# Kernel optimization log

Hardware: AMD Instinct MI355X
Metric: run time of the kernel (lower is better)

Reference implementation:

```python
import jax, jax.numpy as jnp
import numpy as np

EPS = 1e-5
TEMPERATURE = 1.0


def _gn(x, w, b):
    # GroupNorm(dim, dim): num_groups == channels -> per-channel norm over spatial
    mu = x.mean((2, 3), keepdims=True)
    var = x.var((2, 3), keepdims=True)
    return (x - mu) * jax.lax.rsqrt(var + EPS) * w[None, :, None, None] + b[None, :, None, None]


def _deconv(x, w, b):
    # torch ConvTranspose2d(Cin, Cout, 3, stride=2, padding=1, output_padding=1)
    # == dilated conv with lhs_dilation=2, padding (1,2); kernel flip absorbed into random weights
    y = jax.lax.conv_general_dilated(
        x, w, window_strides=(1, 1), padding=((1, 2), (1, 2)),
        lhs_dilation=(2, 2), dimension_numbers=('NCHW', 'OIHW', 'NCHW'))
    return y + b[None, :, None, None]


def _spatial_softmax(logits, temp):
    # logits (..., h, w) -> expected (x, y) coords in [-1, 1], shape (..., 2)
    h, w = logits.shape[-2], logits.shape[-1]
    p = jax.nn.softmax(logits.reshape(*logits.shape[:-2], h * w) / temp, axis=-1)
    ys, xs = jnp.meshgrid(jnp.linspace(-1.0, 1.0, h), jnp.linspace(-1.0, 1.0, w), indexing='ij')
    ex = p @ xs.reshape(-1)
    ey = p @ ys.reshape(-1)
    return jnp.stack([ex, ey], axis=-1)


def setup_inputs() -> dict:
    key = jax.random.key(0)
    ks = iter(jax.random.split(key, 40))
    B, FC, FH = 512, 256, 4   # batch, encoder channels, encoder spatial
    H = 512                   # hidden_size
    STEPS, NHEADS, C = 5, 3, H // 8

    def nrm(shape, scale):
        return jax.random.normal(next(ks), shape, jnp.float32) * scale

    inp = {
        'feat': nrm((B, FC, FH, FH), 1.0),
        'action': jax.random.randint(next(ks), (B,), 0, NHEADS),
        'scene_idx': jax.random.randint(next(ks), (B,), 0, 10),
        'fc_w': nrm((FC, H), (2.0 / FC) ** 0.5),
        'fc_b': jnp.zeros((H,), jnp.float32),
    }
    for i, d in enumerate([512, 256, 128]):
        inp[f'gw{i}'] = jnp.ones((d,), jnp.float32)
        inp[f'gb{i}'] = jnp.zeros((d,), jnp.float32)
        inp[f'dw{i}'] = nrm((d // 2, d, 3, 3), (2.0 / (d * 9)) ** 0.5)
        inp[f'db{i}'] = jnp.zeros((d // 2,), jnp.float32)
    inp['hgw'] = jnp.ones((NHEADS, C), jnp.float32)
    inp['hgb'] = jnp.zeros((NHEADS, C), jnp.float32)
    inp['hcw'] = nrm((NHEADS, STEPS, C), (2.0 / C) ** 0.5)
    inp['hcb'] = jnp.zeros((NHEADS, STEPS), jnp.float32)
    return inp


def reference(feat, action, scene_idx, fc_w, fc_b,
              gw0, gb0, dw0, db0, gw1, gb1, dw1, db1, gw2, gb2, dw2, db2,
              hgw, hgb, hcw, hcb):
    # visual_fc1 applied channel-last == 1x1 linear over channels
    x = jax.nn.relu(jnp.einsum('bchw,cd->bdhw', feat, fc_w) + fc_b[None, :, None, None])
    # deconv stack: (B,512,4,4) -> (B,256,8,8) -> (B,128,16,16) -> (B,64,32,32)
    for gw, gb, dw, db in ((gw0, gb0, dw0, db0), (gw1, gb1, dw1, db1), (gw2, gb2, dw2, db2)):
        x = jax.nn.relu(_deconv(_gn(x, gw, gb), dw, db))
    # expert heads: shared per-channel normalization, head-specific affine fused into 1x1 conv
    mu = x.mean((2, 3), keepdims=True)
    var = x.var((2, 3), keepdims=True)
    xn = (x - mu) * jax.lax.rsqrt(var + EPS)                       # (B,64,32,32)
    w_eff = hcw * hgw[:, None, :]                                  # (A,S,C)
    b_eff = hcb + jnp.einsum('asc,ac->as', hcw, hgb)               # (A,S)
    logits = jnp.einsum('bchw,asc->abshw', xn, w_eff) + b_eff[:, None, :, None, None]
    coords = _spatial_softmax(logits, TEMPERATURE)                 # (A,B,S,2)
    # route each sample to its action's head (== masked scatter loop in torch)
    out = coords[action, jnp.arange(action.shape[0])]              # (B,S,2)
    return out
```

## Files before the change

### kernel.cpp

```cpp
#include <hip/hip_runtime.h>
#include <hip/hip_bf16.h>

#define DI __device__ __forceinline__
using u16 = unsigned short;
using u32 = unsigned int;

typedef short short8 __attribute__((ext_vector_type(8)));
typedef float f32x4 __attribute__((ext_vector_type(4)));

#define F4C(v, i) ((i) == 0 ? (v).x : (i) == 1 ? (v).y : (i) == 2 ? (v).z : (v).w)

DI float bflo(u32 u) { return __uint_as_float(u << 16); }
DI float bfhi(u32 u) { return __uint_as_float(u & 0xffff0000u); }
DI float bfel(uint2 u, int j) { u32 w = (j < 2) ? u.x : u.y; return (j & 1) ? bfhi(w) : bflo(w); }
DI u16 f2bf(float a) {
  u32 xu = __float_as_uint(a);
  return (u16)((xu + 0x7fffu + ((xu >> 16) & 1)) >> 16);
}
DI u32 pack_bf16x2(float a, float b) {
  u32 xu = __float_as_uint(a), yu = __float_as_uint(b);
  xu = (xu + 0x7fffu + ((xu >> 16) & 1)) >> 16;
  yu = (yu + 0x7fffu + ((yu >> 16) & 1)) >> 16;
  return (xu & 0xffffu) | (yu << 16);
}

static constexpr size_t OFF_REGB = 0;
static constexpr size_t OFF_REGA = 16777216;
static constexpr size_t OFF_WT0  = 33554432;
static constexpr size_t OFF_WT1  = OFF_WT0 + 1179648;
static constexpr size_t OFF_WT2  = OFF_WT1 + 294912;
static constexpr size_t OFF_WTF  = OFF_WT2 + 73728;
static constexpr size_t OFF_ST   = 35200000;
static constexpr size_t O_SC0 = OFF_ST,          O_SH0 = OFF_ST + 262144;
static constexpr size_t O_SC1 = OFF_ST + 524288, O_SH1 = OFF_ST + 655360;
static constexpr size_t O_SC2 = OFF_ST + 786432, O_SH2 = OFF_ST + 851968;
static constexpr size_t O_PSUM = OFF_ST + 1048576;

__global__ __launch_bounds__(256)
void wtrans_all(const float* __restrict__ dw0, const float* __restrict__ dw1,
                const float* __restrict__ dw2, const float* __restrict__ fcw,
                u16* __restrict__ wt0, u16* __restrict__ wt1,
                u16* __restrict__ wt2, u16* __restrict__ wtf)
{
  int id = blockIdx.x * 256 + threadIdx.x;
  if (id < 131072) {
    int m = id >> 9, c = id & 511;
    const float* src = dw0 + ((size_t)m * 512 + c) * 9;
#pragma unroll
    for (int tap = 0; tap < 9; ++tap)
      wt0[((size_t)tap * 256 + m) * 512 + c] = f2bf(src[tap]);
  } else if (id < 163840) {
    int j = id - 131072;
    int m = j >> 8, c = j & 255;
    const float* src = dw1 + ((size_t)m * 256 + c) * 9;
#pragma unroll
    for (int tap = 0; tap < 9; ++tap)
      wt1[((size_t)tap * 128 + m) * 256 + c] = f2bf(src[tap]);
  } else if (id < 172032) {
    int j = id - 163840;
    int m = j >> 7, c = j & 127;
    const float* src = dw2 + ((size_t)m * 128 + c) * 9;
#pragma unroll
    for (int tap = 0; tap < 9; ++tap)
      wt2[((size_t)tap * 64 + m) * 128 + c] = f2bf(src[tap]);
  } else {
    int j = id - 172032;
    int d = j >> 8, c = j & 255;
    wtf[j] = f2bf(fcw[c * 512 + d]);
  }
}

DI void fc_stage_A(const float* __restrict__ feat, int b, u16* Ab, int t)
{
#pragma unroll
  for (int it = 0; it < 2; ++it) {
    int idx = t + it * 256;
    int cp = idx >> 2, hw4 = idx & 3;
    int c = cp * 2;
    const float* xp = feat + ((size_t)b * 256 + c) * 16 + hw4 * 4;
    float4 v0 = *(const float4*)xp;
    float4 v1 = *(const float4*)(xp + 16);
    int c64 = c >> 6, jb = (c & 63) >> 3;
#pragma unroll
    for (int j = 0; j < 4; ++j) {
      int hw = hw4 * 4 + j;
      int row = c64 * 16 + hw;
      *(u32*)&Ab[(row << 6) + ((jb ^ (row & 7)) << 3) + (c & 7)] =
          pack_bf16x2(F4C(v0, j), F4C(v1, j));
    }
  }
}

__global__ __launch_bounds__(256, 2)
void fc_mfma(const float* __restrict__ feat, const u16* __restrict__ wtf,
             const float* __restrict__ fb, const float* __restrict__ gw,
             const float* __restrict__ gb, u16* __restrict__ x0,
             float* __restrict__ sc, float* __restrict__ sh)
{
  __shared__ __align__(16) u16 Wl[256 * 64];
  __shared__ __align__(16) u16 Al[2][64 * 64];
  const int t = threadIdx.x;
  const int lane = t & 63, wave = t >> 6;
  const int n15 = lane & 15, kq = lane >> 4;
  const int d0 = blockIdx.x * 64;
  const int b0 = blockIdx.y * 8;

#pragma unroll
  for (int it = 0; it < 8; ++it) {
    int idx = t + it * 256;
    int dl = idx >> 5, jb32 = idx & 31;
    int row = (jb32 >> 3) * 64 + dl, jb = jb32 & 7;
    uint4 v = *(const uint4*)(wtf + (size_t)(d0 + dl) * 256 + jb32 * 8);
    *(uint4*)&Wl[(row << 6) + ((jb ^ (row & 7)) << 3)] = v;
  }
  fc_stage_A(feat, b0, Al[0], t);

  const int dg = d0 + wave * 16 + n15;
  const float bvn = fb[dg];
  const float gwv = gw[dg], gbv = gb[dg];

  for (int bi = 0; bi < 8; ++bi) {
    __syncthreads();
    if (bi + 1 < 8) fc_stage_A(feat, b0 + bi + 1, Al[(bi + 1) & 1], t);

    const u16* A = Al[bi & 1];
    f32x4 acc0 = {0.f, 0.f, 0.f, 0.f}, acc1 = {0.f, 0.f, 0.f, 0.f};
#pragma unroll
    for (int ks = 0; ks < 8; ++ks) {
      int js = ks * 4 + kq;
      int ra = (js >> 3) * 16 + n15;
      int rb = (js >> 3) * 64 + wave * 16 + n15;
      short8 av = *(const short8*)&A[(ra << 6) + (((js & 7) ^ (ra & 7)) << 3)];
      short8 bv = *(const short8*)&Wl[(rb << 6) + (((js & 7) ^ (rb & 7)) << 3)];
      if (ks & 1) acc1 = __builtin_amdgcn_mfma_f32_16x16x32_bf16(av, bv, acc1, 0, 0, 0);
      else        acc0 = __builtin_amdgcn_mfma_f32_16x16x32_bf16(av, bv, acc0, 0, 0, 0);
    }

    int b = b0 + bi;
    float v[4], s = 0.f, s2 = 0.f;
#pragma unroll
    for (int r = 0; r < 4; ++r) {
      v[r] = fmaxf(acc0[r] + acc1[r] + bvn, 0.f);
      s += v[r]; s2 += v[r] * v[r];
    }
    uint2 pk = {pack_bf16x2(v[0], v[1]), pack_bf16x2(v[2], v[3])};
    *(uint2*)&x0[((size_t)b * 512 + dg) * 16 + kq * 4] = pk;
    s  += __shfl_xor(s, 16, 64);  s  += __shfl_xor(s, 32, 64);
    s2 += __shfl_xor(s2, 16, 64); s2 += __shfl_xor(s2, 32, 64);
    if (kq == 0) {
      float mu = s * (1.f / 16.f);
      float var = fmaxf(s2 * (1.f / 16.f) - mu * mu, 0.f);
      float scale = gwv * rsqrtf(var + 1e-5f);
      sc[(size_t)b * 512 + dg] = scale;
      sh[(size_t)b * 512 + dg] = gbv - mu * scale;
    }
  }
}

template<int STAGE>
__global__ __launch_bounds__(256, 3)
void deconv_mfma(const u16* __restrict__ x, const float* __restrict__ sc,
                 const float* __restrict__ sh, const u16* __restrict__ wt,
                 const float* __restrict__ bias, u16* __restrict__ y,
                 const float* __restrict__ gwn, const float* __restrict__ gbn,
                 float* __restrict__ osc, float* __restrict__ osh)
{
  constexpr int CI  = STAGE == 0 ? 512 : 256;
  constexpr int CO  = CI / 2;
  constexpr int H   = STAGE == 0 ? 4 : 8;
  constexpr int S2I = H * H, S2O = 4 * S2I, W2 = 2 * H;
  constexpr int WP  = H + 1;
  constexpr int XROWS = STAGE == 0 ? 100 : 81;
  constexpr int NCH = CI / 64;
  __shared__ __align__(16) u16 Wl[288 * 64];
  __shared__ __align__(16) u16 Xl[XROWS * 64];
  __shared__ float2 sbuf[2][2][16];

  const int t = threadIdx.x;
  const int lane = t & 63, wave = t >> 6;
  const int ms = wave >> 1, ns = wave & 1;
  const int n15 = lane & 15, kq = lane >> 4;

  int m0, b0;
  m0 = blockIdx.x * 32; b0 = (STAGE == 0) ? blockIdx.y * 4 : blockIdx.y;

  int xrow[2];
#pragma unroll
  for (int ni = 0; ni < 2; ++ni) {
    if constexpr (STAGE == 0) xrow[ni] = (ns * 2 + ni) * 25 + (n15 >> 2) * 5 + (n15 & 3);
    else                      xrow[ni] = (2 * (ns * 2 + ni) + (n15 >> 3)) * 9 + (n15 & 7);
  }
  const int am = ms * 16 + n15;

  for (int i = t; i < XROWS * 32; i += 256) ((u32*)Xl)[i] = 0;

  f32x4 acc[2][4];
#pragma unroll
  for (int ni = 0; ni < 2; ++ni)
#pragma unroll
    for (int c = 0; c < 4; ++c) acc[ni][c] = f32x4{0.f, 0.f, 0.f, 0.f};

  for (int ch = 0; ch < NCH; ++ch) {
    const int c0 = ch * 64;
    __syncthreads();

#pragma unroll
    for (int it = 0; it < 9; ++it) {
      int idx = t + it * 256;
      int row = idx >> 3, jb = idx & 7;
      int tap = row >> 5, ml = row & 31;
      uint4 v = *(const uint4*)(wt + ((size_t)(tap * CO + m0 + ml)) * CI + c0 + jb * 8);
      *(uint4*)&Wl[(row << 6) + ((jb ^ (row & 7)) << 3)] = v;
    }

    for (int idx = t; idx < 16 * 32; idx += 256) {
      int q = idx & 15, p = idx >> 4;
      int c = c0 + 2 * p;
      int b, ldr, gpos;
      if constexpr (STAGE == 0) {
        int img = q >> 2, iy = q & 3;
        b = b0 + img; gpos = iy * 4; ldr = img * 25 + iy * 5;
      } else {
        int iy = q >> 1, cq = q & 1;
        b = b0; gpos = iy * 8 + cq * 4; ldr = iy * 9 + cq * 4;
      }
      const u16* xp = x + ((size_t)b * CI + c) * S2I + gpos;
      uint2 q0 = *(const uint2*)xp;
      uint2 q1 = *(const uint2*)(xp + S2I);
      float s0 = sc[(size_t)b * CI + c],     h0 = sh[(size_t)b * CI + c];
      float s1 = sc[(size_t)b * CI + c + 1], h1 = sh[(size_t)b * CI + c + 1];
      int jb = p >> 2, sub = p & 3;
#pragma unroll
      for (int j = 0; j < 4; ++j) {
        int row = ldr + j;
        *(u32*)&Xl[(row << 6) + ((jb ^ (row & 7)) << 3) + sub * 2] =
            pack_bf16x2(bfel(q0, j) * s0 + h0, bfel(q1, j) * s1 + h1);
      }
    }
    __syncthreads();

#pragma unroll
    for (int s = 0; s < 2; ++s) {
      const int js = s * 4 + kq;
      short8 a[9];
#pragma unroll
      for (int tap = 0; tap < 9; ++tap) {
        int row = tap * 32 + am;
        a[tap] = *(const short8*)&Wl[(row << 6) + ((js ^ (row & 7)) << 3)];
      }
#pragma unroll
      for (int ni = 0; ni < 2; ++ni) {
        int r0 = xrow[ni], r1 = r0 + 1, r2 = r0 + WP, r3 = r0 + WP + 1;
        short8 b00 = *(const short8*)&Xl[(r0 << 6) + ((js ^ (r0 & 7)) << 3)];
        short8 b01 = *(const short8*)&Xl[(r1 << 6) + ((js ^ (r1 & 7)) << 3)];
        short8 b10 = *(const short8*)&Xl[(r2 << 6) + ((js ^ (r2 & 7)) << 3)];
        short8 b11 = *(const short8*)&Xl[(r3 << 6) + ((js ^ (r3 & 7)) << 3)];
        acc[ni][0] = __builtin_amdgcn_mfma_f32_16x16x32_bf16(a[4], b00, acc[ni][0], 0, 0, 0);
        acc[ni][1] = __builtin_amdgcn_mfma_f32_16x16x32_bf16(a[3], b00, acc[ni][1], 0, 0, 0);
        acc[ni][1] = __builtin_amdgcn_mfma_f32_16x16x32_bf16(a[5], b01, acc[ni][1], 0, 0, 0);
        acc[ni][2] = __builtin_amdgcn_mfma_f32_16x16x32_bf16(a[1], b00, acc[ni][2], 0, 0, 0);
        acc[ni][2] = __builtin_amdgcn_mfma_f32_16x16x32_bf16(a[7], b10, acc[ni][2], 0, 0, 0);
        acc[ni][3] = __builtin_amdgcn_mfma_f32_16x16x32_bf16(a[0], b00, acc[ni][3], 0, 0, 0);
        acc[ni][3] = __builtin_amdgcn_mfma_f32_16x16x32_bf16(a[2], b01, acc[ni][3], 0, 0, 0);
        acc[ni][3] = __builtin_amdgcn_mfma_f32_16x16x32_bf16(a[6], b10, acc[ni][3], 0, 0, 0);
        acc[ni][3] = __builtin_amdgcn_mfma_f32_16x16x32_bf16(a[8], b11, acc[ni][3], 0, 0, 0);
      }
    }
  }

  float bv[4];
#pragma unroll
  for (int r = 0; r < 4; ++r) bv[r] = bias[m0 + ms * 16 + kq * 4 + r];

  float sr[4] = {0.f, 0.f, 0.f, 0.f}, sr2[4] = {0.f, 0.f, 0.f, 0.f};
#pragma unroll
  for (int ni = 0; ni < 2; ++ni) {
    int b, iy, ix;
    if constexpr (STAGE == 0) { b = b0 + ns * 2 + ni; iy = n15 >> 2; ix = n15 & 3; }
    else                      { b = b0; iy = 2 * (ns * 2 + ni) + (n15 >> 3); ix = n15 & 7; }

    float val[4][4];
#pragma unroll
    for (int cl = 0; cl < 4; ++cl)
#pragma unroll
      for (int r = 0; r < 4; ++r) {
        val[cl][r] = fmaxf(acc[ni][cl][r] + bv[r], 0.f);
        sr[r] += val[cl][r]; sr2[r] += val[cl][r] * val[cl][r];
      }

    if constexpr (STAGE == 0) {
#pragma unroll
      for (int r = 0; r < 4; ++r) {
        int m = m0 + ms * 16 + kq * 4 + r;
        size_t base = ((size_t)b * CO + m) * S2O + (size_t)(2 * iy) * W2 + 2 * ix;
        *(u32*)(y + base)      = pack_bf16x2(val[0][r], val[1][r]);
        *(u32*)(y + base + W2) = pack_bf16x2(val[2][r], val[3][r]);
      }
#pragma unroll
      for (int r = 0; r < 4; ++r) {
#pragma unroll
        for (int off = 1; off <= 8; off <<= 1) {
          sr[r]  += __shfl_xor(sr[r], off, 64);
          sr2[r] += __shfl_xor(sr2[r], off, 64);
        }
      }
      if (n15 == 0) {
#pragma unroll
        for (int r = 0; r < 4; ++r) {
          int m = m0 + ms * 16 + kq * 4 + r;
          float mu = sr[r] * (1.f / 64.f);
          float var = fmaxf(sr2[r] * (1.f / 64.f) - mu * mu, 0.f);
          float scale = gwn[m] * rsqrtf(var + 1e-5f);
          osc[(size_t)b * CO + m] = scale;
          osh[(size_t)b * CO + m] = gbn[m] - mu * scale;
        }
      }
#pragma unroll
      for (int r = 0; r < 4; ++r) { sr[r] = 0.f; sr2[r] = 0.f; }
    } else {
#pragma unroll
      for (int cl = 0; cl < 4; ++cl) {
        int opx = (2 * iy + (cl >> 1)) * 16 + 2 * ix + (cl & 1);
        size_t base = ((size_t)b * 256 + opx) * 128 + m0 + ms * 16 + kq * 4;
        *(u32*)(y + base)     = pack_bf16x2(val[cl][0], val[cl][1]);
        *(u32*)(y + base + 2) = pack_bf16x2(val[cl][2], val[cl][3]);
      }
    }
  }

  if constexpr (STAGE == 1) {
#pragma unroll
    for (int r = 0; r < 4; ++r) {
#pragma unroll
      for (int off = 1; off <= 8; off <<= 1) {
        sr[r]  += __shfl_xor(sr[r], off, 64);
        sr2[r] += __shfl_xor(sr2[r], off, 64);
      }
    }
    __syncthreads();
    if (n15 == 0) {
#pragma unroll
      for (int r = 0; r < 4; ++r) sbuf[ms][ns][kq * 4 + r] = float2{sr[r], sr2[r]};
    }
    __syncthreads();
    if (t < 32) {
      int msx = t >> 4, i = t & 15;
      float2 p0 = sbuf[msx][0][i], p1 = sbuf[msx][1][i];
      float s = p0.x + p1.x, s2 = p0.y + p1.y;
      float mu = s * (1.f / 256.f);
      float var = fmaxf(s2 * (1.f / 256.f) - mu * mu, 0.f);
      int m = m0 + msx * 16 + i;
      float scale = gwn[m] * rsqrtf(var + 1e-5f);
      osc[(size_t)b0 * CO + m] = scale;
      osh[(size_t)b0 * CO + m] = gbn[m] - mu * scale;
    }
  }
}

#define XRD(row) (*(const short8*)&Xl[((row) << 6) + (((js ^ ((row) & 7))) << 3)])
__global__ __launch_bounds__(256, 3)
void deconv2_q(const u16* __restrict__ x, const float* __restrict__ sc,
               const float* __restrict__ sh, const u16* __restrict__ wt,
               const float* __restrict__ bias, u16* __restrict__ y,
               float2* __restrict__ psum)
{
  __shared__ __align__(16) u16 Wl[288 * 64];
  __shared__ __align__(16) u16 Xl[85 * 64];
  __shared__ float sc_l[128], sh_l[128];
  __shared__ float2 sbuf[2][2][16];

  const int t = threadIdx.x;
  const int lane = t & 63, wave = t >> 6;
  const int ms = wave >> 1, ns = wave & 1;
  const int n15 = lane & 15, kq = lane >> 4;
  const int m0 = (blockIdx.x & 1) * 32;
  const int qz = blockIdx.x >> 1;
  const int b  = blockIdx.y;

  if (t < 128) { sc_l[t] = sc[(size_t)b * 128 + t]; sh_l[t] = sh[(size_t)b * 128 + t]; }
  for (int i = t; i < 85 * 32; i += 256) ((u32*)Xl)[i] = 0;

  const int am = ms * 16 + n15;
  const int xr0 = (ns * 2) * 17 + n15;

  f32x4 acc[2][4];
#pragma unroll
  for (int ni = 0; ni < 2; ++ni)
#pragma unroll
    for (int c = 0; c < 4; ++c) acc[ni][c] = f32x4{0.f, 0.f, 0.f, 0.f};

  const int NPX = (qz < 3) ? 80 : 64;
  for (int ch = 0; ch < 2; ++ch) {
    const int c0 = ch * 64;
    __syncthreads();

#pragma unroll
    for (int it = 0; it < 9; ++it) {
      int idx = t + it * 256;
      int row = idx >> 3, jb = idx & 7;
      int tap = row >> 5, ml = row & 31;
      uint4 v = *(const uint4*)(wt + ((size_t)(tap * 64 + m0 + ml)) * 128 + c0 + jb * 8);
      *(uint4*)&Wl[(row << 6) + ((jb ^ (row & 7)) << 3)] = v;
    }

    for (int idx = t; idx < NPX * 8; idx += 256) {
      int pxl = idx >> 3, jb = idx & 7;
      int rl = pxl >> 4, ix = pxl & 15;
      int gpx = (4 * qz + rl) * 16 + ix;
      uint4 q = *(const uint4*)(x + ((size_t)b * 256 + gpx) * 128 + c0 + jb * 8);
      int cb = c0 + jb * 8;
      float f0 = bflo(q.x) * sc_l[cb + 0] + sh_l[cb + 0];
      float f1 = bfhi(q.x) * sc_l[cb + 1] + sh_l[cb + 1];
      float f2 = bflo(q.y) * sc_l[cb + 2] + sh_l[cb + 2];
      float f3 = bfhi(q.y) * sc_l[cb + 3] + sh_l[cb + 3];
      float f4 = bflo(q.z) * sc_l[cb + 4] + sh_l[cb + 4];
      float f5 = bfhi(q.z) * sc_l[cb + 5] + sh_l[cb + 5];
      float f6 = bflo(q.w) * sc_l[cb + 6] + sh_l[cb + 6];
      float f7 = bfhi(q.w) * sc_l[cb + 7] + sh_l[cb + 7];
      uint4 o = {pack_bf16x2(f0, f1), pack_bf16x2(f2, f3),
                 pack_bf16x2(f4, f5), pack_bf16x2(f6, f7)};
      int row = rl * 17 + ix;
      *(uint4*)&Xl[(row << 6) + ((jb ^ (row & 7)) << 3)] = o;
    }
    __syncthreads();

#pragma unroll
    for (int s = 0; s < 2; ++s) {
      const int js = s * 4 + kq;
      short8 a[9];
#pragma unroll
      for (int tap = 0; tap < 9; ++tap) {
        int row = tap * 32 + am;
        a[tap] = *(const short8*)&Wl[(row << 6) + ((js ^ (row & 7)) << 3)];
      }
      short8 B0 = XRD(xr0),      B1 = XRD(xr0 + 1);
      short8 B2 = XRD(xr0 + 17), B3 = XRD(xr0 + 18);
      short8 B4 = XRD(xr0 + 34), B5 = XRD(xr0 + 35);
#pragma unroll
      for (int ni = 0; ni < 2; ++ni) {
        short8 b00 = ni ? B2 : B0, b01 = ni ? B3 : B1;
        short8 b10 = ni ? B4 : B2, b11 = ni ? B5 : B3;
        acc[ni][0] = __builtin_amdgcn_mfma_f32_16x16x32_bf16(a[4], b00, acc[ni][0], 0, 0, 0);
        acc[ni][1] = __builtin_amdgcn_mfma_f32_16x16x32_bf16(a[3], b00, acc[ni][1], 0, 0, 0);
        acc[ni][1] = __builtin_amdgcn_mfma_f32_16x16x32_bf16(a[5], b01, acc[ni][1], 0, 0, 0);
        acc[ni][2] = __builtin_amdgcn_mfma_f32_16x16x32_bf16(a[1], b00, acc[ni][2], 0, 0, 0);
        acc[ni][2] = __builtin_amdgcn_mfma_f32_16x16x32_bf16(a[7], b10, acc[ni][2], 0, 0, 0);
        acc[ni][3] = __builtin_amdgcn_mfma_f32_16x16x32_bf16(a[0], b00, acc[ni][3], 0, 0, 0);
        acc[ni][3] = __builtin_amdgcn_mfma_f32_16x16x32_bf16(a[2], b01, acc[ni][3], 0, 0, 0);
        acc[ni][3] = __builtin_amdgcn_mfma_f32_16x16x32_bf16(a[6], b10, acc[ni][3], 0, 0, 0);
        acc[ni][3] = __builtin_amdgcn_mfma_f32_16x16x32_bf16(a[8], b11, acc[ni][3], 0, 0, 0);
      }
    }
  }

  float bv[4];
#pragma unroll
  for (int r = 0; r < 4; ++r) bv[r] = bias[m0 + ms * 16 + kq * 4 + r];
  float sr[4] = {0.f, 0.f, 0.f, 0.f}, sr2[4] = {0.f, 0.f, 0.f, 0.f};
#pragma unroll
  for (int ni = 0; ni < 2; ++ni) {
    int iy = 4 * qz + ns * 2 + ni, ix = n15;
#pragma unroll
    for (int r = 0; r < 4; ++r) {
      int m = m0 + ms * 16 + kq * 4 + r;
      float v00 = fmaxf(acc[ni][0][r] + bv[r], 0.f);
      float v01 = fmaxf(acc[ni][1][r] + bv[r], 0.f);
      float v10 = fmaxf(acc[ni][2][r] + bv[r], 0.f);
      float v11 = fmaxf(acc[ni][3][r] + bv[r], 0.f);
      size_t base = ((size_t)b * 64 + m) * 1024 + (size_t)(2 * iy) * 32 + 2 * ix;
      *(u32*)(y + base)      = pack_bf16x2(v00, v01);
      *(u32*)(y + base + 32) = pack_bf16x2(v10, v11);
      sr[r]  += v00 + v01 + v10 + v11;
      sr2[r] += v00 * v00 + v01 * v01 + v10 * v10 + v11 * v11;
    }
  }
#pragma unroll
  for (int r = 0; r < 4; ++r) {
#pragma unroll
    for (int off = 1; off <= 8; off <<= 1) {
      sr[r]  += __shfl_xor(sr[r], off, 64);
      sr2[r] += __shfl_xor(sr2[r], off, 64);
    }
  }
  __syncthreads();
  if (n15 == 0) {
#pragma unroll
    for (int r = 0; r < 4; ++r) sbuf[ms][ns][kq * 4 + r] = float2{sr[r], sr2[r]};
  }
  __syncthreads();
  if (t < 32) {
    int msx = t >> 4, i = t & 15;
    float2 p0 = sbuf[msx][0][i], p1 = sbuf[msx][1][i];
    int m = m0 + msx * 16 + i;
    psum[((size_t)b * 64 + m) * 4 + qz] = float2{p0.x + p1.x, p0.y + p1.y};
  }
}

DI float breduce_sum(float v, float* buf) {
#pragma unroll
  for (int off = 32; off; off >>= 1) v += __shfl_xor(v, off, 64);
  if ((threadIdx.x & 63) == 0) buf[threadIdx.x >> 6] = v;
  __syncthreads();
  float r = (buf[0] + buf[1]) + (buf[2] + buf[3]);
  __syncthreads();
  return r;
}
DI float breduce_max(float v, float* buf) {
#pragma unroll
  for (int off = 32; off; off >>= 1) v = fmaxf(v, __shfl_xor(v, off, 64));
  if ((threadIdx.x & 63) == 0) buf[threadIdx.x >> 6] = v;
  __syncthreads();
  float r = fmaxf(fmaxf(buf[0], buf[1]), fmaxf(buf[2], buf[3]));
  __syncthreads();
  return r;
}

__global__ __launch_bounds__(256)
void head_kernel(const u16* __restrict__ x3, const float2* __restrict__ psum,
                 const int* __restrict__ action, const float* __restrict__ hgw,
                 const float* __restrict__ hcw, float* __restrict__ out)
{
  constexpr int C = 64, S = 5, P = 1024;
  const int b = blockIdx.x, t = threadIdx.x;
  const int a = action[b];
  __shared__ float weff[S * C];
  __shared__ float sc_l[C], sh_l[C];
  __shared__ float rbuf[4];
  if (t < C) {
    float s = 0.f, s2 = 0.f;
#pragma unroll
    for (int qz = 0; qz < 4; ++qz) {
      float2 p = psum[((size_t)b * C + t) * 4 + qz];
      s += p.x; s2 += p.y;
    }
    float mu = s * (1.f / 1024.f);
    float var = fmaxf(s2 * (1.f / 1024.f) - mu * mu, 0.f);
    float rstd = rsqrtf(var + 1e-5f);
    sc_l[t] = rstd; sh_l[t] = -mu * rstd;
  }
  for (int j = t; j < S * C; j += 256) {
    int s = j >> 6, c = j & 63;
    weff[j] = hcw[(a * S + s) * C + c] * hgw[a * C + c];
  }
  __syncthreads();

  float L[S][4];
#pragma unroll
  for (int s = 0; s < S; ++s)
#pragma unroll
    for (int k = 0; k < 4; ++k) L[s][k] = 0.f;

  const u32* xb = (const u32*)(x3 + (size_t)b * C * P);
  for (int c = 0; c < C; ++c) {
    float scv = sc_l[c], shv = sh_l[c];
    u32 u0 = xb[c * 512 + t];
    u32 u1 = xb[c * 512 + t + 256];
    float xv[4] = {bflo(u0) * scv + shv, bfhi(u0) * scv + shv,
                   bflo(u1) * scv + shv, bfhi(u1) * scv + shv};
#pragma unroll
    for (int s = 0; s < S; ++s) {
      float wv = weff[s * C + c];
#pragma unroll
      for (int k = 0; k < 4; ++k) L[s][k] += xv[k] * wv;
    }
  }

#pragma unroll
  for (int s = 0; s < S; ++s) {
    float m = fmaxf(fmaxf(L[s][0], L[s][1]), fmaxf(L[s][2], L[s][3]));
    m = breduce_max(m, rbuf);
    float se = 0.f, sx = 0.f, sy = 0.f;
    const int pix[4] = {2 * t, 2 * t + 1, 512 + 2 * t, 512 + 2 * t + 1};
#pragma unroll
    for (int k = 0; k < 4; ++k) {
      int p = pix[k];
      float e = __expf(L[s][k] - m);
      se += e;
      sx += e * ((float)(p & 31) * (2.f / 31.f) - 1.f);
      sy += e * ((float)(p >> 5) * (2.f / 31.f) - 1.f);
    }
    se = breduce_sum(se, rbuf);
    sx = breduce_sum(sx, rbuf);
    sy = breduce_sum(sy, rbuf);
    if (t == 0) {
      out[(b * S + s) * 2 + 0] = sx / se;
      out[(b * S + s) * 2 + 1] = sy / se;
    }
  }
}

extern "C" void kernel_launch(void* const* d_in, const int* in_sizes, int n_in,
                              void* d_out, int out_size, void* d_ws, size_t ws_size,
                              hipStream_t stream)
{
  (void)in_sizes; (void)n_in; (void)out_size; (void)ws_size;
  const float* feat   = (const float*)d_in[0];
  const int*   action = (const int*)d_in[1];
  const float* fc_w = (const float*)d_in[3];
  const float* fc_b = (const float*)d_in[4];
  const float* gw0  = (const float*)d_in[5];
  const float* gb0  = (const float*)d_in[6];
  const float* dw0  = (const float*)d_in[7];
  const float* db0  = (const float*)d_in[8];
  const float* gw1  = (const float*)d_in[9];
  const float* gb1  = (const float*)d_in[10];
  const float* dw1  = (const float*)d_in[11];
  const float* db1  = (const float*)d_in[12];
  const float* gw2  = (const float*)d_in[13];
  const float* gb2  = (const float*)d_in[14];
  const float* dw2  = (const float*)d_in[15];
  const float* db2  = (const float*)d_in[16];
  const float* hgw  = (const float*)d_in[17];
  const float* hcw  = (const float*)d_in[19];

  float* ws = (float*)d_ws;
  u16* x0 = (u16*)(ws + OFF_REGB);
  u16* x2 = (u16*)(ws + OFF_REGB);
  u16* x1 = (u16*)(ws + OFF_REGA);
  u16* x3 = (u16*)(ws + OFF_REGA);
  u16* wt0 = (u16*)(ws + OFF_WT0);
  u16* wt1 = (u16*)(ws + OFF_WT1);
  u16* wt2 = (u16*)(ws + OFF_WT2);
  u16* wtf = (u16*)(ws + OFF_WTF);
  float* sc0 = ws + O_SC0; float* sh0 = ws + O_SH0;
  float* sc1 = ws + O_SC1; float* sh1 = ws + O_SH1;
  float* sc2 = ws + O_SC2; float* sh2 = ws + O_SH2;
  float2* psum = (float2*)(ws + O_PSUM);

  wtrans_all<<<1184, 256, 0, stream>>>(dw0, dw1, dw2, fc_w, wt0, wt1, wt2, wtf);
  fc_mfma<<<dim3(8, 64), 256, 0, stream>>>(feat, wtf, fc_b, gw0, gb0, x0, sc0, sh0);
  deconv_mfma<0><<<dim3(8, 128), 256, 0, stream>>>(x0, sc0, sh0, wt0, db0, x1, gw1, gb1, sc1, sh1);
  deconv_mfma<1><<<dim3(4, 512), 256, 0, stream>>>(x1, sc1, sh1, wt1, db1, x2, gw2, gb2, sc2, sh2);
  deconv2_q<<<dim3(8, 512), 256, 0, stream>>>(x2, sc2, sh2, wt2, db2, x3, psum);
  head_kernel<<<512, 256, 0, stream>>>(x3, psum, action, hgw, hcw, (float*)d_out);
}
```

Before: 266.1 us.

## Retile last deconv to half-image blocks with 16 channels; halve fc batch per block

The final deconv kernel now tiles each block as 16 output channels by half the input image (8 rows), instead of 32 channels by a quarter (4 rows). Each wave handles different rows with the same channel set, which halves the weight staging in LDS, enlarges the input staging, and targets 4 blocks per CU. Partial GroupNorm statistics are reduced over 2 halves instead of 4, and the head kernel is updated to match. Separately, fc_mfma processes 4 batch items per block instead of 8, doubling the grid for more parallelism at the cost of reloading the weight tile more often.

New measurement: 270.1 us. No clear change (+1.5%).

```diff
diff --git a/kernel.cpp b/kernel.cpp
--- a/kernel.cpp
+++ b/kernel.cpp
@@ -103,7 +103,7 @@
   const int lane = t & 63, wave = t >> 6;
   const int n15 = lane & 15, kq = lane >> 4;
   const int d0 = blockIdx.x * 64;
-  const int b0 = blockIdx.y * 8;
+  const int b0 = blockIdx.y * 4;
 
 #pragma unroll
   for (int it = 0; it < 8; ++it) {
@@ -119,9 +119,9 @@
   const float bvn = fb[dg];
   const float gwv = gw[dg], gbv = gb[dg];
 
-  for (int bi = 0; bi < 8; ++bi) {
+  for (int bi = 0; bi < 4; ++bi) {
     __syncthreads();
-    if (bi + 1 < 8) fc_stage_A(feat, b0 + bi + 1, Al[(bi + 1) & 1], t);
+    if (bi + 1 < 4) fc_stage_A(feat, b0 + bi + 1, Al[(bi + 1) & 1], t);
 
     const u16* A = Al[bi & 1];
     f32x4 acc0 = {0.f, 0.f, 0.f, 0.f}, acc1 = {0.f, 0.f, 0.f, 0.f};
@@ -358,30 +358,26 @@
 }
 
 #define XRD(row) (*(const short8*)&Xl[((row) << 6) + (((js ^ ((row) & 7))) << 3)])
-__global__ __launch_bounds__(256, 3)
-void deconv2_q(const u16* __restrict__ x, const float* __restrict__ sc,
+__global__ __launch_bounds__(256, 4)
+void deconv2_h(const u16* __restrict__ x, const float* __restrict__ sc,
                const float* __restrict__ sh, const u16* __restrict__ wt,
                const float* __restrict__ bias, u16* __restrict__ y,
                float2* __restrict__ psum)
 {
-  __shared__ __align__(16) u16 Wl[288 * 64];
-  __shared__ __align__(16) u16 Xl[85 * 64];
+  __shared__ __align__(16) u16 Wl[144 * 64];
+  __shared__ __align__(16) u16 Xl[153 * 64];
   __shared__ float sc_l[128], sh_l[128];
-  __shared__ float2 sbuf[2][2][16];
+  __shared__ float2 sbuf[4][16];
 
   const int t = threadIdx.x;
-  const int lane = t & 63, wave = t >> 6;
-  const int ms = wave >> 1, ns = wave & 1;
+  const int lane = t & 63, wv = t >> 6;
   const int n15 = lane & 15, kq = lane >> 4;
-  const int m0 = (blockIdx.x & 1) * 32;
-  const int qz = blockIdx.x >> 1;
+  const int m0 = (blockIdx.x & 3) * 16;
+  const int h  = blockIdx.x >> 2;
   const int b  = blockIdx.y;
 
   if (t < 128) { sc_l[t] = sc[(size_t)b * 128 + t]; sh_l[t] = sh[(size_t)b * 128 + t]; }
-  for (int i = t; i < 85 * 32; i += 256) ((u32*)Xl)[i] = 0;
-
-  const int am = ms * 16 + n15;
-  const int xr0 = (ns * 2) * 17 + n15;
+  for (int i = t; i < 153 * 32; i += 256) ((u32*)Xl)[i] = 0;
 
   f32x4 acc[2][4];
 #pragma unroll
@@ -389,24 +385,26 @@
 #pragma unroll
     for (int c = 0; c < 4; ++c) acc[ni][c] = f32x4{0.f, 0.f, 0.f, 0.f};
 
-  const int NPX = (qz < 3) ? 80 : 64;
+  const int NPX = (h == 0) ? 144 : 128;
   for (int ch = 0; ch < 2; ++ch) {
     const int c0 = ch * 64;
     __syncthreads();
 
 #pragma unroll
-    for (int it = 0; it < 9; ++it) {
+    for (int it = 0; it < 5; ++it) {
       int idx = t + it * 256;
-      int row = idx >> 3, jb = idx & 7;
-      int tap = row >> 5, ml = row & 31;
-      uint4 v = *(const uint4*)(wt + ((size_t)(tap * 64 + m0 + ml)) * 128 + c0 + jb * 8);
-      *(uint4*)&Wl[(row << 6) + ((jb ^ (row & 7)) << 3)] = v;
+      if (idx < 1152) {
+        int row = idx >> 3, jb = idx & 7;
+        int tap = row >> 4, ml = row & 15;
+        uint4 v = *(const uint4*)(wt + ((size_t)(tap * 64 + m0 + ml)) * 128 + c0 + jb * 8);
+        *(uint4*)&Wl[(row << 6) + ((jb ^ (row & 7)) << 3)] = v;
+      }
     }
 
     for (int idx = t; idx < NPX * 8; idx += 256) {
       int pxl = idx >> 3, jb = idx & 7;
       int rl = pxl >> 4, ix = pxl & 15;
-      int gpx = (4 * qz + rl) * 16 + ix;
+      int gpx = (8 * h + rl) * 16 + ix;
       uint4 q = *(const uint4*)(x + ((size_t)b * 256 + gpx) * 128 + c0 + jb * 8);
       int cb = c0 + jb * 8;
       float f0 = bflo(q.x) * sc_l[cb + 0] + sh_l[cb + 0];
@@ -430,9 +428,10 @@
       short8 a[9];
 #pragma unroll
       for (int tap = 0; tap < 9; ++tap) {
-        int row = tap * 32 + am;
+        int row = tap * 16 + n15;
         a[tap] = *(const short8*)&Wl[(row << 6) + ((js ^ (row & 7)) << 3)];
       }
+      const int xr0 = (wv * 2) * 17 + n15;
       short8 B0 = XRD(xr0),      B1 = XRD(xr0 + 1);
       short8 B2 = XRD(xr0 + 17), B3 = XRD(xr0 + 18);
       short8 B4 = XRD(xr0 + 34), B5 = XRD(xr0 + 35);
@@ -455,14 +454,14 @@
 
   float bv[4];
 #pragma unroll
-  for (int r = 0; r < 4; ++r) bv[r] = bias[m0 + ms * 16 + kq * 4 + r];
+  for (int r = 0; r < 4; ++r) bv[r] = bias[m0 + kq * 4 + r];
   float sr[4] = {0.f, 0.f, 0.f, 0.f}, sr2[4] = {0.f, 0.f, 0.f, 0.f};
 #pragma unroll
   for (int ni = 0; ni < 2; ++ni) {
-    int iy = 4 * qz + ns * 2 + ni, ix = n15;
+    int iy = 8 * h + wv * 2 + ni, ix = n15;
 #pragma unroll
     for (int r = 0; r < 4; ++r) {
-      int m = m0 + ms * 16 + kq * 4 + r;
+      int m = m0 + kq * 4 + r;
       float v00 = fmaxf(acc[ni][0][r] + bv[r], 0.f);
       float v01 = fmaxf(acc[ni][1][r] + bv[r], 0.f);
       float v10 = fmaxf(acc[ni][2][r] + bv[r], 0.f);
@@ -485,14 +484,14 @@
   __syncthreads();
   if (n15 == 0) {
 #pragma unroll
-    for (int r = 0; r < 4; ++r) sbuf[ms][ns][kq * 4 + r] = float2{sr[r], sr2[r]};
+    for (int r = 0; r < 4; ++r) sbuf[wv][kq * 4 + r] = float2{sr[r], sr2[r]};
   }
   __syncthreads();
-  if (t < 32) {
-    int msx = t >> 4, i = t & 15;
-    float2 p0 = sbuf[msx][0][i], p1 = sbuf[msx][1][i];
-    int m = m0 + msx * 16 + i;
-    psum[((size_t)b * 64 + m) * 4 + qz] = float2{p0.x + p1.x, p0.y + p1.y};
+  if (t < 16) {
+    float s = 0.f, s2 = 0.f;
+#pragma unroll
+    for (int w = 0; w < 4; ++w) { s += sbuf[w][t].x; s2 += sbuf[w][t].y; }
+    psum[((size_t)b * 64 + m0 + t) * 2 + h] = float2{s, s2};
   }
 }
 
@@ -527,12 +526,9 @@
   __shared__ float sc_l[C], sh_l[C];
   __shared__ float rbuf[4];
   if (t < C) {
-    float s = 0.f, s2 = 0.f;
-#pragma unroll
-    for (int qz = 0; qz < 4; ++qz) {
-      float2 p = psum[((size_t)b * C + t) * 4 + qz];
-      s += p.x; s2 += p.y;
-    }
+    float2 p0 = psum[((size_t)b * C + t) * 2 + 0];
+    float2 p1 = psum[((size_t)b * C + t) * 2 + 1];
+    float s = p0.x + p1.x, s2 = p0.y + p1.y;
     float mu = s * (1.f / 1024.f);
     float var = fmaxf(s2 * (1.f / 1024.f) - mu * mu, 0.f);
     float rstd = rsqrtf(var + 1e-5f);
@@ -628,9 +624,9 @@
   float2* psum = (float2*)(ws + O_PSUM);
 
   wtrans_all<<<1184, 256, 0, stream>>>(dw0, dw1, dw2, fc_w, wt0, wt1, wt2, wtf);
-  fc_mfma<<<dim3(8, 64), 256, 0, stream>>>(feat, wtf, fc_b, gw0, gb0, x0, sc0, sh0);
+  fc_mfma<<<dim3(8, 128), 256, 0, stream>>>(feat, wtf, fc_b, gw0, gb0, x0, sc0, sh0);
   deconv_mfma<0><<<dim3(8, 128), 256, 0, stream>>>(x0, sc0, sh0, wt0, db0, x1, gw1, gb1, sc1, sh1);
   deconv_mfma<1><<<dim3(4, 512), 256, 0, stream>>>(x1, sc1, sh1, wt1, db1, x2, gw2, gb2, sc2, sh2);
-  deconv2_q<<<dim3(8, 512), 256, 0, stream>>>(x2, sc2, sh2, wt2, db2, x3, psum);
+  deconv2_h<<<dim3(8, 512), 256, 0, stream>>>(x2, sc2, sh2, wt2, db2, x3, psum);
   head_kernel<<<512, 256, 0, stream>>>(x3, psum, action, hgw, hcw, (float*)d_out);
 }
```

## Remap deconv waves to own a spatial tile and both M halves; halve FC batch per block

Applied to the files above, without the earlier changes.

In the first two deconv stages, each wave now takes one image or row-pair of the spatial tile and computes both 16-row output-channel halves, instead of a 2x2 split over M and N. This loads the four X fragments once per k-step and reuses them across both M halves. The cost is reloading 18 weight fragments per wave instead of 9. The per-channel stats reduction moves to a per-wave shared buffer summed across the four waves. Separately, the FC kernel handles 4 samples per block instead of 8 and launches twice as many blocks, giving more parallelism but restaging the weight tile more often.

New measurement: 268.4 us (median of 2 runs). Within noise of the previous version (+0.9%).

```diff
diff --git a/kernel.cpp b/kernel.cpp
--- a/kernel.cpp
+++ b/kernel.cpp
@@ -103,7 +103,7 @@
   const int lane = t & 63, wave = t >> 6;
   const int n15 = lane & 15, kq = lane >> 4;
   const int d0 = blockIdx.x * 64;
-  const int b0 = blockIdx.y * 8;
+  const int b0 = blockIdx.y * 4;
 
 #pragma unroll
   for (int it = 0; it < 8; ++it) {
@@ -119,9 +119,9 @@
   const float bvn = fb[dg];
   const float gwv = gw[dg], gbv = gb[dg];
 
-  for (int bi = 0; bi < 8; ++bi) {
+  for (int bi = 0; bi < 4; ++bi) {
     __syncthreads();
-    if (bi + 1 < 8) fc_stage_A(feat, b0 + bi + 1, Al[(bi + 1) & 1], t);
+    if (bi + 1 < 4) fc_stage_A(feat, b0 + bi + 1, Al[(bi + 1) & 1], t);
 
     const u16* A = Al[bi & 1];
     f32x4 acc0 = {0.f, 0.f, 0.f, 0.f}, acc1 = {0.f, 0.f, 0.f, 0.f};
@@ -174,31 +174,27 @@
   constexpr int NCH = CI / 64;
   __shared__ __align__(16) u16 Wl[288 * 64];
   __shared__ __align__(16) u16 Xl[XROWS * 64];
-  __shared__ float2 sbuf[2][2][16];
+  __shared__ float2 sbuf[4][32];
 
   const int t = threadIdx.x;
-  const int lane = t & 63, wave = t >> 6;
-  const int ms = wave >> 1, ns = wave & 1;
+  const int lane = t & 63, wv = t >> 6;
   const int n15 = lane & 15, kq = lane >> 4;
 
-  int m0, b0;
-  m0 = blockIdx.x * 32; b0 = (STAGE == 0) ? blockIdx.y * 4 : blockIdx.y;
-
-  int xrow[2];
-#pragma unroll
-  for (int ni = 0; ni < 2; ++ni) {
-    if constexpr (STAGE == 0) xrow[ni] = (ns * 2 + ni) * 25 + (n15 >> 2) * 5 + (n15 & 3);
-    else                      xrow[ni] = (2 * (ns * 2 + ni) + (n15 >> 3)) * 9 + (n15 & 7);
-  }
-  const int am = ms * 16 + n15;
+  const int m0 = blockIdx.x * 32;
+  const int b0 = (STAGE == 0) ? blockIdx.y * 4 : blockIdx.y;
+  const int b  = (STAGE == 0) ? b0 + wv : b0;
+
+  int xrow;
+  if constexpr (STAGE == 0) xrow = wv * 25 + (n15 >> 2) * 5 + (n15 & 3);
+  else                      xrow = (2 * wv + (n15 >> 3)) * 9 + (n15 & 7);
 
   for (int i = t; i < XROWS * 32; i += 256) ((u32*)Xl)[i] = 0;
 
   f32x4 acc[2][4];
 #pragma unroll
-  for (int ni = 0; ni < 2; ++ni)
-#pragma unroll
-    for (int c = 0; c < 4; ++c) acc[ni][c] = f32x4{0.f, 0.f, 0.f, 0.f};
+  for (int mi = 0; mi < 2; ++mi)
+#pragma unroll
+    for (int c = 0; c < 4; ++c) acc[mi][c] = f32x4{0.f, 0.f, 0.f, 0.f};
 
   for (int ch = 0; ch < NCH; ++ch) {
     const int c0 = ch * 64;
@@ -216,19 +212,19 @@
     for (int idx = t; idx < 16 * 32; idx += 256) {
       int q = idx & 15, p = idx >> 4;
       int c = c0 + 2 * p;
-      int b, ldr, gpos;
+      int bb, ldr, gpos;
       if constexpr (STAGE == 0) {
         int img = q >> 2, iy = q & 3;
-        b = b0 + img; gpos = iy * 4; ldr = img * 25 + iy * 5;
+        bb = b0 + img; gpos = iy * 4; ldr = img * 25 + iy * 5;
       } else {
         int iy = q >> 1, cq = q & 1;
-        b = b0; gpos = iy * 8 + cq * 4; ldr = iy * 9 + cq * 4;
-      }
-      const u16* xp = x + ((size_t)b * CI + c) * S2I + gpos;
+        bb = b0; gpos = iy * 8 + cq * 4; ldr = iy * 9 + cq * 4;
+      }
+      const u16* xp = x + ((size_t)bb * CI + c) * S2I + gpos;
       uint2 q0 = *(const uint2*)xp;
       uint2 q1 = *(const uint2*)(xp + S2I);
-      float s0 = sc[(size_t)b * CI + c],     h0 = sh[(size_t)b * CI + c];
-      float s1 = sc[(size_t)b * CI + c + 1], h1 = sh[(size_t)b * CI + c + 1];
+      float s0 = sc[(size_t)bb * CI + c],     h0 = sh[(size_t)bb * CI + c];
+      float s1 = sc[(size_t)bb * CI + c + 1], h1 = sh[(size_t)bb * CI + c + 1];
       int jb = p >> 2, sub = p & 3;
 #pragma unroll
       for (int j = 0; j < 4; ++j) {
@@ -242,56 +238,52 @@
 #pragma unroll
     for (int s = 0; s < 2; ++s) {
       const int js = s * 4 + kq;
-      short8 a[9];
-#pragma unroll
-      for (int tap = 0; tap < 9; ++tap) {
-        int row = tap * 32 + am;
-        a[tap] = *(const short8*)&Wl[(row << 6) + ((js ^ (row & 7)) << 3)];
-      }
-#pragma unroll
-      for (int ni = 0; ni < 2; ++ni) {
-        int r0 = xrow[ni], r1 = r0 + 1, r2 = r0 + WP, r3 = r0 + WP + 1;
-        short8 b00 = *(const short8*)&Xl[(r0 << 6) + ((js ^ (r0 & 7)) << 3)];
-        short8 b01 = *(const short8*)&Xl[(r1 << 6) + ((js ^ (r1 & 7)) << 3)];
-        short8 b10 = *(const short8*)&Xl[(r2 << 6) + ((js ^ (r2 & 7)) << 3)];
-        short8 b11 = *(const short8*)&Xl[(r3 << 6) + ((js ^ (r3 & 7)) << 3)];
-        acc[ni][0] = __builtin_amdgcn_mfma_f32_16x16x32_bf16(a[4], b00, acc[ni][0], 0, 0, 0);
-        acc[ni][1] = __builtin_amdgcn_mfma_f32_16x16x32_bf16(a[3], b00, acc[ni][1], 0, 0, 0);
-        acc[ni][1] = __builtin_amdgcn_mfma_f32_16x16x32_bf16(a[5], b01, acc[ni][1], 0, 0, 0);
-        acc[ni][2] = __builtin_amdgcn_mfma_f32_16x16x32_bf16(a[1], b00, acc[ni][2], 0, 0, 0);
-        acc[ni][2] = __builtin_amdgcn_mfma_f32_16x16x32_bf16(a[7], b10, acc[ni][2], 0, 0, 0);
-        acc[ni][3] = __builtin_amdgcn_mfma_f32_16x16x32_bf16(a[0], b00, acc[ni][3], 0, 0, 0);
-        acc[ni][3] = __builtin_amdgcn_mfma_f32_16x16x32_bf16(a[2], b01, acc[ni][3], 0, 0, 0);
-        acc[ni][3] = __builtin_amdgcn_mfma_f32_16x16x32_bf16(a[6], b10, acc[ni][3], 0, 0, 0);
-        acc[ni][3] = __builtin_amdgcn_mfma_f32_16x16x32_bf16(a[8], b11, acc[ni][3], 0, 0, 0);
-      }
-    }
-  }
-
-  float bv[4];
-#pragma unroll
-  for (int r = 0; r < 4; ++r) bv[r] = bias[m0 + ms * 16 + kq * 4 + r];
-
-  float sr[4] = {0.f, 0.f, 0.f, 0.f}, sr2[4] = {0.f, 0.f, 0.f, 0.f};
-#pragma unroll
-  for (int ni = 0; ni < 2; ++ni) {
-    int b, iy, ix;
-    if constexpr (STAGE == 0) { b = b0 + ns * 2 + ni; iy = n15 >> 2; ix = n15 & 3; }
-    else                      { b = b0; iy = 2 * (ns * 2 + ni) + (n15 >> 3); ix = n15 & 7; }
-
+      const int r0 = xrow, r1 = r0 + 1, r2 = r0 + WP, r3 = r0 + WP + 1;
+      short8 b00 = *(const short8*)&Xl[(r0 << 6) + ((js ^ (r0 & 7)) << 3)];
+      short8 b01 = *(const short8*)&Xl[(r1 << 6) + ((js ^ (r1 & 7)) << 3)];
+      short8 b10 = *(const short8*)&Xl[(r2 << 6) + ((js ^ (r2 & 7)) << 3)];
+      short8 b11 = *(const short8*)&Xl[(r3 << 6) + ((js ^ (r3 & 7)) << 3)];
+#pragma unroll
+      for (int mi = 0; mi < 2; ++mi) {
+        short8 a[9];
+#pragma unroll
+        for (int tap = 0; tap < 9; ++tap) {
+          int row = tap * 32 + mi * 16 + n15;
+          a[tap] = *(const short8*)&Wl[(row << 6) + ((js ^ (row & 7)) << 3)];
+        }
+        acc[mi][0] = __builtin_amdgcn_mfma_f32_16x16x32_bf16(a[4], b00, acc[mi][0], 0, 0, 0);
+        acc[mi][1] = __builtin_amdgcn_mfma_f32_16x16x32_bf16(a[3], b00, acc[mi][1], 0, 0, 0);
+        acc[mi][1] = __builtin_amdgcn_mfma_f32_16x16x32_bf16(a[5], b01, acc[mi][1], 0, 0, 0);
+        acc[mi][2] = __builtin_amdgcn_mfma_f32_16x16x32_bf16(a[1], b00, acc[mi][2], 0, 0, 0);
+        acc[mi][2] = __builtin_amdgcn_mfma_f32_16x16x32_bf16(a[7], b10, acc[mi][2], 0, 0, 0);
+        acc[mi][3] = __builtin_amdgcn_mfma_f32_16x16x32_bf16(a[0], b00, acc[mi][3], 0, 0, 0);
+        acc[mi][3] = __builtin_amdgcn_mfma_f32_16x16x32_bf16(a[2], b01, acc[mi][3], 0, 0, 0);
+        acc[mi][3] = __builtin_amdgcn_mfma_f32_16x16x32_bf16(a[6], b10, acc[mi][3], 0, 0, 0);
+        acc[mi][3] = __builtin_amdgcn_mfma_f32_16x16x32_bf16(a[8], b11, acc[mi][3], 0, 0, 0);
+      }
+    }
+  }
+
+#pragma unroll
+  for (int mi = 0; mi < 2; ++mi) {
+    float bvv[4];
+#pragma unroll
+    for (int r = 0; r < 4; ++r) bvv[r] = bias[m0 + mi * 16 + kq * 4 + r];
     float val[4][4];
+    float sr[4] = {0.f, 0.f, 0.f, 0.f}, sr2[4] = {0.f, 0.f, 0.f, 0.f};
 #pragma unroll
     for (int cl = 0; cl < 4; ++cl)
 #pragma unroll
       for (int r = 0; r < 4; ++r) {
-        val[cl][r] = fmaxf(acc[ni][cl][r] + bv[r], 0.f);
+        val[cl][r] = fmaxf(acc[mi][cl][r] + bvv[r], 0.f);
         sr[r] += val[cl][r]; sr2[r] += val[cl][r] * val[cl][r];
       }
 
     if constexpr (STAGE == 0) {
+      int iy = n15 >> 2, ix = n15 & 3;
 #pragma unroll
       for (int r = 0; r < 4; ++r) {
-        int m = m0 + ms * 16 + kq * 4 + r;
+        int m = m0 + mi * 16 + kq * 4 + r;
         size_t base = ((size_t)b * CO + m) * S2O + (size_t)(2 * iy) * W2 + 2 * ix;
         *(u32*)(y + base)      = pack_bf16x2(val[0][r], val[1][r]);
         *(u32*)(y + base + W2) = pack_bf16x2(val[2][r], val[3][r]);
@@ -307,7 +299,7 @@
       if (n15 == 0) {
 #pragma unroll
         for (int r = 0; r < 4; ++r) {
-          int m = m0 + ms * 16 + kq * 4 + r;
+          int m = m0 + mi * 16 + kq * 4 + r;
           float mu = sr[r] * (1.f / 64.f);
           float var = fmaxf(sr2[r] * (1.f / 64.f) - mu * mu, 0.f);
           float scale = gwn[m] * rsqrtf(var + 1e-5f);
@@ -315,41 +307,39 @@
           osh[(size_t)b * CO + m] = gbn[m] - mu * scale;
         }
       }
-#pragma unroll
-      for (int r = 0; r < 4; ++r) { sr[r] = 0.f; sr2[r] = 0.f; }
     } else {
+      int iy = 2 * wv + (n15 >> 3), ix = n15 & 7;
 #pragma unroll
       for (int cl = 0; cl < 4; ++cl) {
         int opx = (2 * iy + (cl >> 1)) * 16 + 2 * ix + (cl & 1);
-        size_t base = ((size_t)b * 256 + opx) * 128 + m0 + ms * 16 + kq * 4;
+        size_t base = ((size_t)b * 256 + opx) * 128 + m0 + mi * 16 + kq * 4;
         *(u32*)(y + base)     = pack_bf16x2(val[cl][0], val[cl][1]);
         *(u32*)(y + base + 2) = pack_bf16x2(val[cl][2], val[cl][3]);
       }
+#pragma unroll
+      for (int r = 0; r < 4; ++r) {
+#pragma unroll
+        for (int off = 1; off <= 8; off <<= 1) {
+          sr[r]  += __shfl_xor(sr[r], off, 64);
+          sr2[r] += __shfl_xor(sr2[r], off, 64);
+        }
+      }
+      if (n15 == 0) {
+#pragma unroll
+        for (int r = 0; r < 4; ++r) sbuf[wv][mi * 16 + kq * 4 + r] = float2{sr[r], sr2[r]};
+      }
     }
   }
 
   if constexpr (STAGE == 1) {
-#pragma unroll
-    for (int r = 0; r < 4; ++r) {
-#pragma unroll
-      for (int off = 1; off <= 8; off <<= 1) {
-        sr[r]  += __shfl_xor(sr[r], off, 64);
-        sr2[r] += __shfl_xor(sr2[r], off, 64);
-      }
-    }
-    __syncthreads();
-    if (n15 == 0) {
-#pragma unroll
-      for (int r = 0; r < 4; ++r) sbuf[ms][ns][kq * 4 + r] = float2{sr[r], sr2[r]};
-    }
     __syncthreads();
     if (t < 32) {
-      int msx = t >> 4, i = t & 15;
-      float2 p0 = sbuf[msx][0][i], p1 = sbuf[msx][1][i];
-      float s = p0.x + p1.x, s2 = p0.y + p1.y;
+      float s = 0.f, s2 = 0.f;
+#pragma unroll
+      for (int w = 0; w < 4; ++w) { s += sbuf[w][t].x; s2 += sbuf[w][t].y; }
       float mu = s * (1.f / 256.f);
       float var = fmaxf(s2 * (1.f / 256.f) - mu * mu, 0.f);
-      int m = m0 + msx * 16 + i;
+      int m = m0 + t;
       float scale = gwn[m] * rsqrtf(var + 1e-5f);
       osc[(size_t)b0 * CO + m] = scale;
       osh[(size_t)b0 * CO + m] = gbn[m] - mu * scale;
@@ -628,7 +618,7 @@
   float2* psum = (float2*)(ws + O_PSUM);
 
   wtrans_all<<<1184, 256, 0, stream>>>(dw0, dw1, dw2, fc_w, wt0, wt1, wt2, wtf);
-  fc_mfma<<<dim3(8, 64), 256, 0, stream>>>(feat, wtf, fc_b, gw0, gb0, x0, sc0, sh0);
+  fc_mfma<<<dim3(8, 128), 256, 0, stream>>>(feat, wtf, fc_b, gw0, gb0, x0, sc0, sh0);
   deconv_mfma<0><<<dim3(8, 128), 256, 0, stream>>>(x0, sc0, sh0, wt0, db0, x1, gw1, gb1, sc1, sh1);
   deconv_mfma<1><<<dim3(4, 512), 256, 0, stream>>>(x1, sc1, sh1, wt1, db1, x2, gw2, gb2, sc2, sh2);
   deconv2_q<<<dim3(8, 512), 256, 0, stream>>>(x2, sc2, sh2, wt2, db2, x3, psum);
```
